# Optimization experiments

Measured on AMD Instinct MI355X. Metric: run time of the kernel, lower is better.

The kernel has to match this reference:

```python
import jax, jax.numpy as jnp
import numpy as np

NUM_EXPERTS = 64
NOISE_STD = 1.0
CAPACITY = 32  # top-C items per expert (experts-choice routing)
D_MODEL = 512
NUM_GROUPS = 8
GROUP_SIZE = 2048


def _top_items_per_expert_dispatcher(gates):
    """Experts-choice dispatcher for one group.

    gates: (S, E) softmax gate values.
    Returns:
      dispatch: (E, C, S) one-hot selection of the top-C items per expert.
      combine:  (S, E, C) gate value if item s is expert e's c-th pick, else 0.
    """
    s = gates.shape[0]
    # Each expert picks its top-C items by gate value.
    _, top_idx = jax.lax.top_k(gates.T, CAPACITY)          # (E, C)
    dispatch = jax.nn.one_hot(top_idx, s, dtype=gates.dtype)  # (E, C, S)
    combine = jnp.einsum('se,ecs->sec', gates, dispatch)      # (S, E, C)
    return dispatch, combine


def setup_inputs() -> dict:
    key = jax.random.key(0)
    k1, k2 = jax.random.split(key)
    inputs = jax.random.normal(k1, (NUM_GROUPS, GROUP_SIZE, D_MODEL), dtype=jnp.float32)
    # Dense(num_experts, use_bias=False) kernel, lecun-normal-ish scale.
    W = jax.random.normal(k2, (D_MODEL, NUM_EXPERTS), dtype=jnp.float32) * (D_MODEL ** -0.5)
    return {"inputs": inputs, "W": W}


def reference(inputs, W):
    # Gating projection: (G, S, D) x (D, E) -> (G, S, E)
    logits = jnp.einsum('gsd,de->gse', inputs, W)
    # Noisy gating: noise_std scaled by 1/num_experts (as in the module).
    noise_scale = NOISE_STD / NUM_EXPERTS
    noise = noise_scale * jax.random.normal(jax.random.key(42), logits.shape, dtype=logits.dtype)
    gates = jax.nn.softmax(logits + noise, axis=-1)  # (G, S, E)
    # vmap the per-group top-items-per-expert dispatcher over groups.
    dispatch, combine = jax.vmap(_top_items_per_expert_dispatcher)(gates)
    return combine, dispatch
```

## Files before the change

### kernel.cpp

```cpp
#include <hip/hip_runtime.h>
#include <math.h>
#include <stdint.h>

#define NG 8
#define GS 2048
#define DM 512
#define NE 64
#define CAP 32
#define NROWS (NG * GS)
#define COMBINE_ELEMS (33554432ull)

#define GATE_BLOCKS 512
#define XST 516
#define TBS 21

typedef float f32x4 __attribute__((ext_vector_type(4)));
typedef double f64x2 __attribute__((ext_vector_type(2)));
typedef double f64x4 __attribute__((ext_vector_type(4)));
typedef unsigned long long u64;

__device__ __forceinline__ void threefry2x32(uint32_t k0, uint32_t k1,
                                             uint32_t x0, uint32_t x1,
                                             uint32_t& o0, uint32_t& o1) {
  uint32_t ks[3] = {k0, k1, k0 ^ k1 ^ 0x1BD11BDAu};
  x0 += ks[0];
  x1 += ks[1];
  const uint32_t rot[2][4] = {{13u, 15u, 26u, 6u}, {17u, 29u, 16u, 24u}};
#pragma unroll
  for (int i = 0; i < 5; ++i) {
#pragma unroll
    for (int j = 0; j < 4; ++j) {
      uint32_t r = rot[i & 1][j];
      x0 += x1;
      x1 = (x1 << r) | (x1 >> (32u - r));
      x1 ^= x0;
    }
    x0 += ks[(i + 1) % 3];
    x1 += ks[(i + 2) % 3] + (uint32_t)(i + 1);
  }
  o0 = x0;
  o1 = x1;
}

__device__ __forceinline__ float erfinv_xla(float x) {
  float w = -log1pf(-x * x);
  float p;
  if (w < 5.0f) {
    w = w - 2.5f;
    p = 2.81022636e-08f;
    p = __fmaf_rn(p, w, 3.43273939e-07f);
    p = __fmaf_rn(p, w, -3.5233877e-06f);
    p = __fmaf_rn(p, w, -4.39150654e-06f);
    p = __fmaf_rn(p, w, 0.00021858087f);
    p = __fmaf_rn(p, w, -0.00125372503f);
    p = __fmaf_rn(p, w, -0.00417768164f);
    p = __fmaf_rn(p, w, 0.246640727f);
    p = __fmaf_rn(p, w, 1.50140941f);
  } else {
    w = sqrtf(w) - 3.0f;
    p = -0.000200214257f;
    p = __fmaf_rn(p, w, 0.000100950558f);
    p = __fmaf_rn(p, w, 0.00134934322f);
    p = __fmaf_rn(p, w, -0.00367342844f);
    p = __fmaf_rn(p, w, 0.00573950773f);
    p = __fmaf_rn(p, w, -0.0076224613f);
    p = __fmaf_rn(p, w, 0.00943887047f);
    p = __fmaf_rn(p, w, 1.00167406f);
    p = __fmaf_rn(p, w, 2.83297682f);
  }
  return p * x;
}

__device__ __forceinline__ float jax_normal(uint32_t idx) {
  uint32_t o0, o1;
  threefry2x32(0u, 42u, 0u, idx, o0, o1);
  uint32_t bits = o0 ^ o1;
  float f = __uint_as_float((bits >> 9) | 0x3f800000u) - 1.0f;
  const float lo = __uint_as_float(0xBF7FFFFFu);
  float v = fmaxf(lo, f * 2.0f + lo);
  return __uint_as_float(0x3FB504F3u) * erfinv_xla(v);
}

__global__ __launch_bounds__(256) void wprep_kernel(
    const float* __restrict__ Wt, double* __restrict__ Wd) {
  const int i = blockIdx.x * 256 + threadIdx.x;
  const int t = i & 3, i15 = (i >> 2) & 15, row = i >> 6;
  Wd[i] = (double)Wt[row * NE + t * 16 + i15];
}

__global__ __launch_bounds__(128) void gate_kernel(
    const float* __restrict__ x,
    const double* __restrict__ Wd,
    float* __restrict__ gatesT) {
  __shared__ float xs[32 * XST];
  const int gid = blockIdx.x;
  const int tid = threadIdx.x;
  const int l = tid & 63;
  const int w = tid >> 6;
  const int row0b = gid * 32;
  const int row0 = row0b + w * 16;

  const int i15 = l & 15;
  const int k4 = l >> 4;

  f64x4 dr = {0., 0., 0., 0.};
  dr = __builtin_amdgcn_mfma_f64_16x16x4f64((double)i15, 0.25, dr, 0, 0, 0);
  int perm[4];
#pragma unroll
  for (int r = 0; r < 4; ++r) perm[r] = ((int)(dr[r] + 0.5)) & 15;

#pragma unroll 8
  for (int i = tid; i < 4096; i += 128) {
    const int r = i >> 7, c = (i & 127) << 2;
    *(f32x4*)&xs[r * XST + c] =
        *(const f32x4*)&x[(size_t)(row0b + r) * DM + c];
  }
  __syncthreads();

  f64x4 acc[4] = {{0., 0., 0., 0.}, {0., 0., 0., 0.},
                  {0., 0., 0., 0.}, {0., 0., 0., 0.}};
  const float* xrow = &xs[(w * 16 + i15) * XST + k4];
  const double* wl = Wd + k4 * 64 + i15 * 4;
  f64x2 b01 = *(const f64x2*)(wl + 0);
  f64x2 b23 = *(const f64x2*)(wl + 2);
#pragma unroll 4
  for (int kk = 0; kk < 128; ++kk) {
    const int nk = (kk + 1) & 127;
    const f64x2 nb01 = *(const f64x2*)(wl + nk * 256 + 0);
    const f64x2 nb23 = *(const f64x2*)(wl + nk * 256 + 2);
    const double a = (double)xrow[kk * 4];
    acc[0] = __builtin_amdgcn_mfma_f64_16x16x4f64(a, b01[0], acc[0], 0, 0, 0);
    acc[1] = __builtin_amdgcn_mfma_f64_16x16x4f64(a, b01[1], acc[1], 0, 0, 0);
    acc[2] = __builtin_amdgcn_mfma_f64_16x16x4f64(a, b23[0], acc[2], 0, 0, 0);
    acc[3] = __builtin_amdgcn_mfma_f64_16x16x4f64(a, b23[1], acc[3], 0, 0, 0);
    b01 = nb01;
    b23 = nb23;
  }

  float gatef[4][4];
#pragma unroll
  for (int r = 0; r < 4; ++r) {
    const int row = row0 + perm[r];
    double v[4];
    double m = -1.0e300;
#pragma unroll
    for (int t = 0; t < 4; ++t) {
      const float logit = (float)acc[t][r];
      const float noised =
          logit + 0.015625f * jax_normal((uint32_t)(row * NE + 16 * t + i15));
      v[t] = (double)noised;
      m = fmax(m, v[t]);
    }
#pragma unroll
    for (int off = 1; off < 16; off <<= 1) m = fmax(m, __shfl_xor(m, off, 64));
    double s = 0.0;
#pragma unroll
    for (int t = 0; t < 4; ++t) {
      v[t] = exp(v[t] - m);
      s += v[t];
    }
#pragma unroll
    for (int off = 1; off < 16; off <<= 1) s += __shfl_xor(s, off, 64);
#pragma unroll
    for (int t = 0; t < 4; ++t) gatef[t][r] = (float)(v[t] / s);
  }

  float* tb = xs + w * (NE * TBS);
#pragma unroll
  for (int t = 0; t < 4; ++t)
#pragma unroll
    for (int r = 0; r < 4; ++r)
      tb[(16 * t + i15) * TBS + perm[r]] = gatef[t][r];

  const int g = row0 >> 11;
  const int s0 = row0 & (GS - 1);
  float* drow = gatesT + ((size_t)(g * NE + l)) * GS + s0;
#pragma unroll
  for (int c = 0; c < 4; ++c) {
    f32x4 o;
#pragma unroll
    for (int i = 0; i < 4; ++i) o[i] = tb[l * TBS + 4 * c + i];
    *(f32x4*)&drow[4 * c] = o;
  }
}

__global__ __launch_bounds__(64) void topsel_kernel(
    const float* __restrict__ gatesT,
    u64* __restrict__ topsel) {
  const int ge = blockIdx.x;
  const int lane = threadIdx.x;

  const float* base = gatesT + (size_t)ge * GS;
  u64 K[32];
#pragma unroll
  for (int k = 0; k < 8; ++k) {
    const f32x4 t = *(const f32x4*)(base + k * 256 + lane * 4);
#pragma unroll
    for (int i = 0; i < 4; ++i) {
      const int s = k * 256 + lane * 4 + i;
      K[k * 4 + i] = ((u64)__float_as_uint(t[i]) << 32) | (u64)(2047 - s);
    }
  }

#pragma unroll
  for (int k = 2; k <= 32; k <<= 1) {
#pragma unroll
    for (int d = k >> 1; d > 0; d >>= 1) {
#pragma unroll
      for (int j = 0; j < 32; ++j) {
        const int ixj = j ^ d;
        if (ixj > j) {
          const bool asc = ((j & k) == 0);
          const u64 a = K[j], b = K[ixj];
          const bool sw = asc ? (a > b) : (a < b);
          K[j] = sw ? b : a;
          K[ixj] = sw ? a : b;
        }
      }
    }
  }

#pragma unroll
  for (int m = 1; m < 64; m <<= 1) {
    u64 tmp[32];
#pragma unroll
    for (int j = 0; j < 32; ++j) tmp[j] = __shfl_xor(K[31 - j], m, 64);
#pragma unroll
    for (int j = 0; j < 32; ++j) K[j] = (K[j] > tmp[j]) ? K[j] : tmp[j];
#pragma unroll
    for (int d = 16; d > 0; d >>= 1) {
#pragma unroll
      for (int j = 0; j < 32; ++j) {
        if ((j & d) == 0) {
          const u64 a = K[j], b = K[j | d];
          const bool sw = (a > b);
          K[j] = sw ? b : a;
          K[j | d] = sw ? a : b;
        }
      }
    }
  }

#pragma unroll
  for (int c = 0; c < CAP; ++c) {
    if (lane == c) topsel[(size_t)ge * CAP + c] = K[31 - c];
  }
}

__global__ __launch_bounds__(256) void writer_kernel(
    const u64* __restrict__ topsel,
    float* __restrict__ out) {
  __shared__ int sel_s[CAP];
  __shared__ float sel_v[CAP];
  __shared__ unsigned char c_of_s[GS];
  const int b = blockIdx.x;
  const int ge = b >> 2, q = b & 3;
  const int g = ge >> 6, e = ge & 63;
  const int tid = threadIdx.x;
  const int lane = tid & 63, w = tid >> 6;

  ((u64*)c_of_s)[tid] = ~0ull;
  if (tid < CAP) {
    const u64 key = topsel[(size_t)ge * CAP + tid];
    sel_s[tid] = 2047 - (int)(key & 0x7FFull);
    sel_v[tid] = __uint_as_float((uint32_t)(key >> 32));
  }
  __syncthreads();
  if (tid < CAP) c_of_s[sel_s[tid]] = (unsigned char)tid;
  __syncthreads();

  float* drow_base = out + COMBINE_ELEMS + (size_t)ge * CAP * GS;
#pragma unroll
  for (int rr = 0; rr < 2; ++rr) {
    const int c = 8 * q + 2 * w + rr;
    const int sc = sel_s[c];
    float* rowp = drow_base + (size_t)c * GS;
#pragma unroll
    for (int j = 0; j < 8; ++j) {
      const int pos = j * 256 + lane * 4;
      f32x4 v;
      v[0] = (sc == pos + 0) ? 1.0f : 0.0f;
      v[1] = (sc == pos + 1) ? 1.0f : 0.0f;
      v[2] = (sc == pos + 2) ? 1.0f : 0.0f;
      v[3] = (sc == pos + 3) ? 1.0f : 0.0f;
      *(f32x4*)&rowp[pos] = v;
    }
  }

  const int pos = (lane & 7) * 4;
#pragma unroll
  for (int it = 0; it < 16; ++it) {
    const int s = 512 * q + 128 * w + 8 * it + (lane >> 3);
    const int c = c_of_s[s];
    const float val = (c != 255) ? sel_v[c & 31] : 0.0f;
    const int d = c - pos;
    f32x4 v;
    v[0] = (d == 0) ? val : 0.0f;
    v[1] = (d == 1) ? val : 0.0f;
    v[2] = (d == 2) ? val : 0.0f;
    v[3] = (d == 3) ? val : 0.0f;
    *(f32x4*)&out[(((size_t)(g * GS + s)) * NE + e) * CAP + pos] = v;
  }
}

extern "C" void kernel_launch(void* const* d_in, const int* in_sizes, int n_in,
                              void* d_out, int out_size, void* d_ws,
                              size_t ws_size, hipStream_t stream) {
  (void)in_sizes; (void)n_in; (void)ws_size; (void)out_size;
  const float* x = (const float*)d_in[0];
  const float* Wt = (const float*)d_in[1];
  float* out = (float*)d_out;
  float* gatesT = (float*)d_ws;
  double* Wd = (double*)((char*)d_ws + ((size_t)NROWS * NE * 4));
  u64* topsel = (u64*)((char*)Wd + (size_t)DM * NE * 8);

  wprep_kernel<<<128, 256, 0, stream>>>(Wt, Wd);
  gate_kernel<<<GATE_BLOCKS, 128, 0, stream>>>(x, Wd, gatesT);
  topsel_kernel<<<NG * NE, 64, 0, stream>>>(gatesT, topsel);
  writer_kernel<<<NG * NE * 4, 256, 0, stream>>>(topsel, out);
}
```

Baseline: 119.4 us.

## Split gate-kernel K loop across two wave pairs with shared-memory reduction

Doubles the gate kernel block from 128 to 256 threads. Each pair of waves now handles one half of the 512-long reduction dimension, so the serial chain of f64 MFMAs per wave is half as long. The upper-half waves write their partial accumulators to shared memory, and the lower-half waves add them in before doing softmax and the transpose store. This adds two block barriers and extra shared-memory traffic, and it slightly changes the f64 summation order.

New measurement: 119.9 us. About the same (+0.3%).

```diff
diff --git a/kernel.cpp b/kernel.cpp
--- a/kernel.cpp
+++ b/kernel.cpp
@@ -88,7 +88,7 @@
   Wd[i] = (double)Wt[row * NE + t * 16 + i15];
 }
 
-__global__ __launch_bounds__(128) void gate_kernel(
+__global__ __launch_bounds__(256) void gate_kernel(
     const float* __restrict__ x,
     const double* __restrict__ Wd,
     float* __restrict__ gatesT) {
@@ -96,9 +96,11 @@
   const int gid = blockIdx.x;
   const int tid = threadIdx.x;
   const int l = tid & 63;
-  const int w = tid >> 6;
+  const int w4 = tid >> 6;
+  const int wr = w4 & 1;
+  const int kh = w4 >> 1;
   const int row0b = gid * 32;
-  const int row0 = row0b + w * 16;
+  const int row0 = row0b + wr * 16;
 
   const int i15 = l & 15;
   const int k4 = l >> 4;
@@ -110,7 +112,7 @@
   for (int r = 0; r < 4; ++r) perm[r] = ((int)(dr[r] + 0.5)) & 15;
 
 #pragma unroll 8
-  for (int i = tid; i < 4096; i += 128) {
+  for (int i = tid; i < 4096; i += 256) {
     const int r = i >> 7, c = (i & 127) << 2;
     *(f32x4*)&xs[r * XST + c] =
         *(const f32x4*)&x[(size_t)(row0b + r) * DM + c];
@@ -119,15 +121,16 @@
 
   f64x4 acc[4] = {{0., 0., 0., 0.}, {0., 0., 0., 0.},
                   {0., 0., 0., 0.}, {0., 0., 0., 0.}};
-  const float* xrow = &xs[(w * 16 + i15) * XST + k4];
+  const float* xrow = &xs[(wr * 16 + i15) * XST + k4];
   const double* wl = Wd + k4 * 64 + i15 * 4;
-  f64x2 b01 = *(const f64x2*)(wl + 0);
-  f64x2 b23 = *(const f64x2*)(wl + 2);
+  const int kk0 = kh * 64;
+  f64x2 b01 = *(const f64x2*)(wl + (size_t)kk0 * 256 + 0);
+  f64x2 b23 = *(const f64x2*)(wl + (size_t)kk0 * 256 + 2);
 #pragma unroll 4
-  for (int kk = 0; kk < 128; ++kk) {
+  for (int kk = kk0; kk < kk0 + 64; ++kk) {
     const int nk = (kk + 1) & 127;
-    const f64x2 nb01 = *(const f64x2*)(wl + nk * 256 + 0);
-    const f64x2 nb23 = *(const f64x2*)(wl + nk * 256 + 2);
+    const f64x2 nb01 = *(const f64x2*)(wl + (size_t)nk * 256 + 0);
+    const f64x2 nb23 = *(const f64x2*)(wl + (size_t)nk * 256 + 2);
     const double a = (double)xrow[kk * 4];
     acc[0] = __builtin_amdgcn_mfma_f64_16x16x4f64(a, b01[0], acc[0], 0, 0, 0);
     acc[1] = __builtin_amdgcn_mfma_f64_16x16x4f64(a, b01[1], acc[1], 0, 0, 0);
@@ -136,6 +139,26 @@
     b01 = nb01;
     b23 = nb23;
   }
+  __syncthreads();
+
+  double* pd = (double*)&xs[4096];
+  if (kh == 1) {
+    double* dst = pd + ((size_t)(wr * 64 + l)) * 16;
+#pragma unroll
+    for (int t = 0; t < 4; ++t)
+#pragma unroll
+      for (int r = 0; r < 4; ++r) dst[t * 4 + r] = acc[t][r];
+  }
+  __syncthreads();
+  if (kh == 1) return;
+
+  {
+    const double* src = pd + ((size_t)(wr * 64 + l)) * 16;
+#pragma unroll
+    for (int t = 0; t < 4; ++t)
+#pragma unroll
+      for (int r = 0; r < 4; ++r) acc[t][r] += src[t * 4 + r];
+  }
 
   float gatef[4][4];
 #pragma unroll
@@ -165,7 +188,7 @@
     for (int t = 0; t < 4; ++t) gatef[t][r] = (float)(v[t] / s);
   }
 
-  float* tb = xs + w * (NE * TBS);
+  float* tb = xs + wr * (NE * TBS);
 #pragma unroll
   for (int t = 0; t < 4; ++t)
 #pragma unroll
@@ -315,7 +338,7 @@
   u64* topsel = (u64*)((char*)Wd + (size_t)DM * NE * 8);
 
   wprep_kernel<<<128, 256, 0, stream>>>(Wt, Wd);
-  gate_kernel<<<GATE_BLOCKS, 128, 0, stream>>>(x, Wd, gatesT);
+  gate_kernel<<<GATE_BLOCKS, 256, 0, stream>>>(x, Wd, gatesT);
   topsel_kernel<<<NG * NE, 64, 0, stream>>>(gatesT, topsel);
   writer_kernel<<<NG * NE * 4, 256, 0, stream>>>(topsel, out);
 }
```
